# Performance work log

Hardware: AMD Instinct MI355X
Metric: run time of the kernel (lower is better)

The kernel has to match this reference:

```python
import jax, jax.numpy as jnp
import numpy as np

NUM_ANCHORS = 3
MAX_DETECTIONS = 10
CONF_THRESH = 0.5


def setup_inputs() -> dict:
    key = jax.random.key(0)
    k1, k2, k3 = jax.random.split(key, 3)
    B, T, D = 32, 512, 2048
    features = jax.random.normal(k1, (B, T, D), dtype=jnp.float32)
    W_bbox = jax.random.normal(k2, (D, NUM_ANCHORS * 4), dtype=jnp.float32) * 0.02
    b_bbox = jnp.zeros((NUM_ANCHORS * 4,), dtype=jnp.float32)
    W_conf = jax.random.normal(k3, (D, NUM_ANCHORS), dtype=jnp.float32) * 0.02
    b_conf = jnp.zeros((NUM_ANCHORS,), dtype=jnp.float32)
    return {"features": features, "W_bbox": W_bbox, "b_bbox": b_bbox,
            "W_conf": W_conf, "b_conf": b_conf}


def reference(features, W_bbox, b_bbox, W_conf, b_conf):
    # features: [B, T, D]
    B, T, D = features.shape
    A = NUM_ANCHORS
    k = min(MAX_DETECTIONS, A)  # = 3

    # Dual linear heads (the two trivial GEMMs)
    bbox_pred = (jnp.einsum('btd,df->btf', features, W_bbox) + b_bbox).reshape(B, T, A, 4)
    conf_pred = jax.nn.sigmoid(jnp.einsum('btd,da->bta', features, W_conf) + b_conf)  # [B,T,A]

    # Vectorized replacement of the per-(b,t) Python loop:
    # top-k over anchors, gather boxes, threshold mask -> padded output.
    topk_conf, topk_idx = jax.lax.top_k(conf_pred, k)                    # [B,T,k]
    topk_boxes = jnp.take_along_axis(bbox_pred, topk_idx[..., None], axis=2)  # [B,T,k,4]
    valid = topk_conf > CONF_THRESH                                      # [B,T,k]
    # Invalid slots zeroed: matches the original's "drop invalid / zeros fallback"
    # semantics in a fixed-shape padded representation.
    boxes_out = jnp.where(valid[..., None], topk_boxes, 0.0)
    return boxes_out, topk_conf, valid
```

## Files before the change

kernel.cpp:

```cpp
#include <hip/hip_runtime.h>
#include <math.h>


#define DCOLS 2048
#define RPB   64
#define NW    16
#define CHUNK (DCOLS / NW)
#define PSTR  15

__global__ __launch_bounds__(1024, 4)
void ped_det_kernel(const float* __restrict__ feat,
                    const float* __restrict__ Wb,
                    const float* __restrict__ bb,
                    const float* __restrict__ Wc,
                    const float* __restrict__ bc,
                    float* __restrict__ out,
                    int nrows)
{
    __shared__ float P[NW * RPB * PSTR];
    float* S = P;

    const int t    = threadIdx.x;
    const int lane = t & 63;
    const int w    = t >> 6;
    const int wu   = __builtin_amdgcn_readfirstlane(w);
    const int row  = blockIdx.x * RPB + lane;
    const int kb   = wu * CHUNK;

    float acc[15];
#pragma unroll
    for (int j = 0; j < 15; ++j) acc[j] = 0.0f;

    const float* fp = feat + (size_t)row * DCOLS;

#pragma unroll
    for (int g = 0; g < CHUNK / 16; ++g) {
        const int d0 = kb + g * 16;
        const float4 f0 = *(const float4*)(fp + d0 + 0);
        const float4 f1 = *(const float4*)(fp + d0 + 4);
        const float4 f2 = *(const float4*)(fp + d0 + 8);
        const float4 f3 = *(const float4*)(fp + d0 + 12);
        const float fv[16] = { f0.x, f0.y, f0.z, f0.w,
                               f1.x, f1.y, f1.z, f1.w,
                               f2.x, f2.y, f2.z, f2.w,
                               f3.x, f3.y, f3.z, f3.w };
#pragma unroll
        for (int q = 0; q < 4; ++q) {
            const int du = d0 + q * 4;
            const float* __restrict__ wbp = Wb + (size_t)du * 12;
            const float* __restrict__ wcp = Wc + (size_t)du * 3;
#pragma unroll
            for (int j = 0; j < 4; ++j) {
                const float v = fv[q * 4 + j];
                acc[0]  += v * wbp[j * 12 + 0];
                acc[1]  += v * wbp[j * 12 + 1];
                acc[2]  += v * wbp[j * 12 + 2];
                acc[3]  += v * wbp[j * 12 + 3];
                acc[4]  += v * wbp[j * 12 + 4];
                acc[5]  += v * wbp[j * 12 + 5];
                acc[6]  += v * wbp[j * 12 + 6];
                acc[7]  += v * wbp[j * 12 + 7];
                acc[8]  += v * wbp[j * 12 + 8];
                acc[9]  += v * wbp[j * 12 + 9];
                acc[10] += v * wbp[j * 12 + 10];
                acc[11] += v * wbp[j * 12 + 11];
                acc[12] += v * wcp[j * 3 + 0];
                acc[13] += v * wcp[j * 3 + 1];
                acc[14] += v * wcp[j * 3 + 2];
            }
        }
    }

    {
        float* pp = &P[(wu * RPB + lane) * PSTR];
#pragma unroll
        for (int j = 0; j < 15; ++j) pp[j] = acc[j];
    }
    __syncthreads();

    float sval = 0.0f;
    int rl = 0, jj = 0;
    if (t < RPB * 15) {
        rl = t / 15;
        jj = t % 15;
        float s = 0.0f;
#pragma unroll
        for (int w2 = 0; w2 < NW; ++w2)
            s += P[(w2 * RPB + rl) * PSTR + jj];
        s += (jj < 12) ? bb[jj] : bc[jj - 12];
        sval = s;
    }
    __syncthreads();

    if (t < RPB * 15)
        S[rl * 16 + jj] = sval;
    __syncthreads();

    if (t < RPB) {
        const int r2 = t;
        float box[12];
#pragma unroll
        for (int j = 0; j < 12; ++j) box[j] = S[r2 * 16 + j];
        float conf[3];
#pragma unroll
        for (int a = 0; a < 3; ++a)
            conf[a] = 1.0f / (1.0f + __expf(-S[r2 * 16 + 12 + a]));

        int i0 = 0; float m0 = conf[0];
        if (conf[1] > m0) { i0 = 1; m0 = conf[1]; }
        if (conf[2] > m0) { i0 = 2; m0 = conf[2]; }
        const int ra = (i0 == 0) ? 1 : 0;
        const int rb = (i0 == 2) ? 1 : 2;
        int i1, i2;
        if (conf[rb] > conf[ra]) { i1 = rb; i2 = ra; }
        else                     { i1 = ra; i2 = rb; }
        const int idx[3] = { i0, i1, i2 };

        const int ro = blockIdx.x * RPB + r2;
        float* boxout  = out + (size_t)ro * 12;
        float* confout = out + (size_t)nrows * 12 + (size_t)ro * 3;
        float* valout  = out + (size_t)nrows * 15 + (size_t)ro * 3;
#pragma unroll
        for (int sl = 0; sl < 3; ++sl) {
            const int   a   = idx[sl];
            const float cv  = conf[a];
            const bool  vld = cv > 0.5f;
            float4 bx;
            bx.x = vld ? box[a * 4 + 0] : 0.0f;
            bx.y = vld ? box[a * 4 + 1] : 0.0f;
            bx.z = vld ? box[a * 4 + 2] : 0.0f;
            bx.w = vld ? box[a * 4 + 3] : 0.0f;
            *(float4*)(boxout + sl * 4) = bx;
            confout[sl] = cv;
            valout[sl]  = vld ? 1.0f : 0.0f;
        }
    }
}

extern "C" void kernel_launch(void* const* d_in, const int* in_sizes, int n_in,
                              void* d_out, int out_size, void* d_ws, size_t ws_size,
                              hipStream_t stream) {
    const float* feat = (const float*)d_in[0];
    const float* Wb   = (const float*)d_in[1];
    const float* bb   = (const float*)d_in[2];
    const float* Wc   = (const float*)d_in[3];
    const float* bc   = (const float*)d_in[4];
    float* out = (float*)d_out;

    const int nrows   = in_sizes[0] / DCOLS;
    const int nblocks = nrows / RPB;

    ped_det_kernel<<<dim3(nblocks), dim3(1024), 0, stream>>>(
        feat, Wb, bb, Wc, bc, out, nrows);
}
```

Baseline: 40.59 us.

## Split-K GEMV with double-buffered global-to-LDS staging and separate epilogue kernel

Splits the feature reduction dimension in half across two blocks per 64-row tile, staging features through a swizzled double-buffered LDS tile loaded with direct global-to-LDS async loads. Partial sums go to workspace and a second kernel adds them, applies bias and sigmoid, and does the top-k selection and writes. The aim is coalesced, latency-hidden streaming of the 128MB feature tensor and more blocks in flight. The cost is an extra launch, a workspace round trip, and barriers on every chunk.

```diff
diff --git a/kernel.cpp b/kernel.cpp
--- a/kernel.cpp
+++ b/kernel.cpp
@@ -1,57 +1,79 @@
 #include <hip/hip_runtime.h>
 #include <math.h>
+#include <stdint.h>
 
 
 #define DCOLS 2048
 #define RPB   64
-#define NW    16
-#define CHUNK (DCOLS / NW)
-#define PSTR  15
+#define NWAVE 8
+#define KHALF 1024
+#define CCH   64
+#define NCH   (KHALF / CCH)
+#define TILEF (RPB * CCH)
 
-__global__ __launch_bounds__(1024, 4)
-void ped_det_kernel(const float* __restrict__ feat,
-                    const float* __restrict__ Wb,
-                    const float* __restrict__ bb,
-                    const float* __restrict__ Wc,
-                    const float* __restrict__ bc,
-                    float* __restrict__ out,
-                    int nrows)
+__global__ __launch_bounds__(512, 4)
+void ped_part_kernel(const float* __restrict__ feat,
+                     const float* __restrict__ Wb,
+                     const float* __restrict__ Wc,
+                     float* __restrict__ ws)
 {
-    __shared__ float P[NW * RPB * PSTR];
-    float* S = P;
+    __shared__ __align__(16) float lds[2][TILEF];
 
     const int t    = threadIdx.x;
     const int lane = t & 63;
     const int w    = t >> 6;
     const int wu   = __builtin_amdgcn_readfirstlane(w);
-    const int row  = blockIdx.x * RPB + lane;
-    const int kb   = wu * CHUNK;
+
+    const int half    = blockIdx.x & 1;
+    const int rowBase = (blockIdx.x >> 1) * RPB;
+    const int kbase   = half * KHALF;
+
+    const int rsub = lane >> 4;
+    const int su   = lane & 15;
 
     float acc[15];
 #pragma unroll
     for (int j = 0; j < 15; ++j) acc[j] = 0.0f;
 
-    const float* fp = feat + (size_t)row * DCOLS;
+    const float* fbase = feat + (size_t)rowBase * DCOLS + kbase;
 
+    auto STAGE = [&](int c, int p) {
 #pragma unroll
-    for (int g = 0; g < CHUNK / 16; ++g) {
-        const int d0 = kb + g * 16;
-        const float4 f0 = *(const float4*)(fp + d0 + 0);
-        const float4 f1 = *(const float4*)(fp + d0 + 4);
-        const float4 f2 = *(const float4*)(fp + d0 + 8);
-        const float4 f3 = *(const float4*)(fp + d0 + 12);
-        const float fv[16] = { f0.x, f0.y, f0.z, f0.w,
-                               f1.x, f1.y, f1.z, f1.w,
-                               f2.x, f2.y, f2.z, f2.w,
-                               f3.x, f3.y, f3.z, f3.w };
+        for (int i = 0; i < 2; ++i) {
+            const int r  = wu * 8 + i * 4 + rsub;
+            const int gs = su ^ (r & 7);
+            const float* g = fbase + (size_t)r * DCOLS + c * CCH + gs * 4;
+            const float* l = &lds[p][(wu * 8 + i * 4) * CCH];
+            __builtin_amdgcn_global_load_lds(
+                (const __attribute__((address_space(1))) void*)g,
+                (__attribute__((address_space(3))) void*)l, 16, 0, 0);
+        }
+    };
+
+    STAGE(0, 0);
+
+    for (int c = 0; c < NCH; ++c) {
+        if (c + 1 < NCH) {
+            STAGE(c + 1, (c + 1) & 1);
+            asm volatile("s_waitcnt vmcnt(2)" ::: "memory");
+        } else {
+            asm volatile("s_waitcnt vmcnt(0)" ::: "memory");
+        }
+        asm volatile("s_barrier" ::: "memory");
+
+        const float* buf = &lds[c & 1][0];
 #pragma unroll
-        for (int q = 0; q < 4; ++q) {
-            const int du = d0 + q * 4;
+        for (int q = 0; q < 2; ++q) {
+            const int s = wu * 2 + q;
+            const float4 f = *(const float4*)(buf + (size_t)lane * CCH
+                                              + ((s ^ (lane & 7)) << 2));
+            const int du = kbase + c * CCH + wu * 8 + q * 4;
             const float* __restrict__ wbp = Wb + (size_t)du * 12;
             const float* __restrict__ wcp = Wc + (size_t)du * 3;
+            const float fv[4] = { f.x, f.y, f.z, f.w };
 #pragma unroll
             for (int j = 0; j < 4; ++j) {
-                const float v = fv[q * 4 + j];
+                const float v = fv[j];
                 acc[0]  += v * wbp[j * 12 + 0];
                 acc[1]  += v * wbp[j * 12 + 1];
                 acc[2]  += v * wbp[j * 12 + 2];
@@ -69,71 +91,84 @@
                 acc[14] += v * wcp[j * 3 + 2];
             }
         }
+        asm volatile("s_waitcnt lgkmcnt(0)" ::: "memory");
+        asm volatile("s_barrier" ::: "memory");
     }
 
     {
-        float* pp = &P[(wu * RPB + lane) * PSTR];
+        float* P  = &lds[0][0];
+        float* pp = P + (size_t)(wu * RPB + lane) * 16;
 #pragma unroll
         for (int j = 0; j < 15; ++j) pp[j] = acc[j];
     }
     __syncthreads();
 
-    float sval = 0.0f;
-    int rl = 0, jj = 0;
-    if (t < RPB * 15) {
-        rl = t / 15;
-        jj = t % 15;
-        float s = 0.0f;
+    const float* P = &lds[0][0];
 #pragma unroll
-        for (int w2 = 0; w2 < NW; ++w2)
-            s += P[(w2 * RPB + rl) * PSTR + jj];
-        s += (jj < 12) ? bb[jj] : bc[jj - 12];
-        sval = s;
+    for (int u0 = 0; u0 < 2; ++u0) {
+        const int u = t + u0 * 512;
+        if (u < RPB * 15) {
+            const int r = u / 15;
+            const int j = u - r * 15;
+            float sum = 0.0f;
+#pragma unroll
+            for (int w2 = 0; w2 < NWAVE; ++w2)
+                sum += P[(size_t)(w2 * RPB + r) * 16 + j];
+            ws[((size_t)(rowBase + r) * 2 + half) * 16 + j] = sum;
+        }
     }
-    __syncthreads();
+}
 
-    if (t < RPB * 15)
-        S[rl * 16 + jj] = sval;
-    __syncthreads();
+__global__ __launch_bounds__(256, 4)
+void ped_epi_kernel(const float* __restrict__ ws,
+                    const float* __restrict__ bb,
+                    const float* __restrict__ bc,
+                    float* __restrict__ out, int nrows)
+{
+    const int r = blockIdx.x * 256 + threadIdx.x;
+    if (r >= nrows) return;
 
-    if (t < RPB) {
-        const int r2 = t;
-        float box[12];
+    const float* p = ws + (size_t)r * 32;
+    float s[15];
 #pragma unroll
-        for (int j = 0; j < 12; ++j) box[j] = S[r2 * 16 + j];
-        float conf[3];
+    for (int j = 0; j < 15; ++j)
+        s[j] = p[j] + p[16 + j] + ((j < 12) ? bb[j] : bc[j - 12]);
+
+    float conf[3];
 #pragma unroll
-        for (int a = 0; a < 3; ++a)
-            conf[a] = 1.0f / (1.0f + __expf(-S[r2 * 16 + 12 + a]));
+    for (int a = 0; a < 3; ++a)
+        conf[a] = 1.0f / (1.0f + __expf(-s[12 + a]));
 
-        int i0 = 0; float m0 = conf[0];
-        if (conf[1] > m0) { i0 = 1; m0 = conf[1]; }
-        if (conf[2] > m0) { i0 = 2; m0 = conf[2]; }
-        const int ra = (i0 == 0) ? 1 : 0;
-        const int rb = (i0 == 2) ? 1 : 2;
-        int i1, i2;
-        if (conf[rb] > conf[ra]) { i1 = rb; i2 = ra; }
-        else                     { i1 = ra; i2 = rb; }
-        const int idx[3] = { i0, i1, i2 };
+    int i0 = 0; float m0 = conf[0];
+    if (conf[1] > m0) { i0 = 1; m0 = conf[1]; }
+    if (conf[2] > m0) { i0 = 2; m0 = conf[2]; }
+    const int ra = (i0 == 0) ? 1 : 0;
+    const int rb = (i0 == 2) ? 1 : 2;
+    int i1, i2;
+    if (conf[rb] > conf[ra]) { i1 = rb; i2 = ra; }
+    else                     { i1 = ra; i2 = rb; }
+    const int idx[3] = { i0, i1, i2 };
 
-        const int ro = blockIdx.x * RPB + r2;
-        float* boxout  = out + (size_t)ro * 12;
-        float* confout = out + (size_t)nrows * 12 + (size_t)ro * 3;
-        float* valout  = out + (size_t)nrows * 15 + (size_t)ro * 3;
+    float* boxout  = out + (size_t)r * 12;
+    float* confout = out + (size_t)nrows * 12 + (size_t)r * 3;
+    float* valout  = out + (size_t)nrows * 15 + (size_t)r * 3;
 #pragma unroll
-        for (int sl = 0; sl < 3; ++sl) {
-            const int   a   = idx[sl];
-            const float cv  = conf[a];
-            const bool  vld = cv > 0.5f;
-            float4 bx;
-            bx.x = vld ? box[a * 4 + 0] : 0.0f;
-            bx.y = vld ? box[a * 4 + 1] : 0.0f;
-            bx.z = vld ? box[a * 4 + 2] : 0.0f;
-            bx.w = vld ? box[a * 4 + 3] : 0.0f;
-            *(float4*)(boxout + sl * 4) = bx;
-            confout[sl] = cv;
-            valout[sl]  = vld ? 1.0f : 0.0f;
-        }
+    for (int sl = 0; sl < 3; ++sl) {
+        const int   a   = idx[sl];
+        const float cv  = conf[a];
+        const bool  vld = cv > 0.5f;
+        const float b0 = (a == 0) ? s[0] : (a == 1) ? s[4]  : s[8];
+        const float b1 = (a == 0) ? s[1] : (a == 1) ? s[5]  : s[9];
+        const float b2 = (a == 0) ? s[2] : (a == 1) ? s[6]  : s[10];
+        const float b3 = (a == 0) ? s[3] : (a == 1) ? s[7]  : s[11];
+        float4 bx;
+        bx.x = vld ? b0 : 0.0f;
+        bx.y = vld ? b1 : 0.0f;
+        bx.z = vld ? b2 : 0.0f;
+        bx.w = vld ? b3 : 0.0f;
+        *(float4*)(boxout + sl * 4) = bx;
+        confout[sl] = cv;
+        valout[sl]  = vld ? 1.0f : 0.0f;
     }
 }
 
@@ -146,10 +181,12 @@
     const float* Wc   = (const float*)d_in[3];
     const float* bc   = (const float*)d_in[4];
     float* out = (float*)d_out;
+    float* ws  = (float*)d_ws;
 
-    const int nrows   = in_sizes[0] / DCOLS;
-    const int nblocks = nrows / RPB;
+    const int nrows = in_sizes[0] / DCOLS;
+    const int nb1   = (nrows / RPB) * 2;
 
-    ped_det_kernel<<<dim3(nblocks), dim3(1024), 0, stream>>>(
-        feat, Wb, bb, Wc, bc, out, nrows);
+    ped_part_kernel<<<dim3(nb1), dim3(512), 0, stream>>>(feat, Wb, Wc, ws);
+    ped_epi_kernel<<<dim3((nrows + 255) / 256), dim3(256), 0, stream>>>(
+        ws, bb, bc, out, nrows);
 }
```

Result: no change. 41.10 us (+1.2%).

## Stage feature tiles through LDS with async global_load_lds multi-buffering

Applied to the files above, without the earlier changes.

Replaces each lane's direct strided float4 loads of its own row with a 4-deep LDS ring of 64x64 tiles filled by global_load_lds. Each wave copies four rows coalesced, using an XOR swizzle, then reads its 4-column slice back from LDS. Manual vmcnt waits and barriers are meant to overlap the next tiles' loads with the current FMAs. In exchange it adds two block barriers per chunk across 32 chunks, raises LDS use to 64KB, which may cut occupancy, and re-reads weights with smaller per-iteration work.

```diff
diff --git a/kernel.cpp b/kernel.cpp
--- a/kernel.cpp
+++ b/kernel.cpp
@@ -1,11 +1,15 @@
 #include <hip/hip_runtime.h>
 #include <math.h>
+#include <stdint.h>
 
 
 #define DCOLS 2048
 #define RPB   64
 #define NW    16
-#define CHUNK (DCOLS / NW)
+#define CCH   64
+#define NCH   (DCOLS / CCH)
+#define NBUF  4
+#define TILEF (RPB * CCH)
 #define PSTR  15
 
 __global__ __launch_bounds__(1024, 4)
@@ -17,58 +21,80 @@
                     float* __restrict__ out,
                     int nrows)
 {
-    __shared__ float P[NW * RPB * PSTR];
+    __shared__ __align__(16) float lds[NBUF][TILEF];
+    float* P = &lds[0][0];
     float* S = P;
 
     const int t    = threadIdx.x;
     const int lane = t & 63;
     const int w    = t >> 6;
     const int wu   = __builtin_amdgcn_readfirstlane(w);
-    const int row  = blockIdx.x * RPB + lane;
-    const int kb   = wu * CHUNK;
+
+    const int rowBase = blockIdx.x * RPB;
+
+    const int rsub = lane >> 4;
+    const int su   = lane & 15;
+    const int rst  = wu * 4 + rsub;
+    const size_t gofs = (size_t)rst * DCOLS + ((su ^ (rst & 7)) << 2);
+    const float* fbase = feat + (size_t)rowBase * DCOLS;
+
+    auto STAGE = [&](int c, int p) {
+        const float* g = fbase + gofs + c * CCH;
+        const float* l = &lds[p][wu * 4 * CCH];
+        __builtin_amdgcn_global_load_lds(
+            (const __attribute__((address_space(1))) void*)g,
+            (__attribute__((address_space(3))) void*)l, 16, 0, 0);
+    };
+
+    const int roff = lane * CCH + ((wu ^ (lane & 7)) << 2);
 
     float acc[15];
 #pragma unroll
     for (int j = 0; j < 15; ++j) acc[j] = 0.0f;
 
-    const float* fp = feat + (size_t)row * DCOLS;
+    STAGE(0, 0);
+    STAGE(1, 1);
+    STAGE(2, 2);
 
+    for (int c = 0; c < NCH; ++c) {
+        if (c + 3 < NCH) STAGE(c + 3, (c + 3) & (NBUF - 1));
+
+        const int rem = NCH - 1 - c;
+        if (rem >= 3)      asm volatile("s_waitcnt vmcnt(3)" ::: "memory");
+        else if (rem == 2) asm volatile("s_waitcnt vmcnt(2)" ::: "memory");
+        else if (rem == 1) asm volatile("s_waitcnt vmcnt(1)" ::: "memory");
+        else               asm volatile("s_waitcnt vmcnt(0)" ::: "memory");
+        asm volatile("s_barrier" ::: "memory");
+
+        const float* buf = &lds[c & (NBUF - 1)][0];
+        const float4 f = *(const float4*)(buf + roff);
+
+        const int du = c * CCH + wu * 4;
+        const float* __restrict__ wbp = Wb + (size_t)du * 12;
+        const float* __restrict__ wcp = Wc + (size_t)du * 3;
+        const float fv[4] = { f.x, f.y, f.z, f.w };
 #pragma unroll
-    for (int g = 0; g < CHUNK / 16; ++g) {
-        const int d0 = kb + g * 16;
-        const float4 f0 = *(const float4*)(fp + d0 + 0);
-        const float4 f1 = *(const float4*)(fp + d0 + 4);
-        const float4 f2 = *(const float4*)(fp + d0 + 8);
-        const float4 f3 = *(const float4*)(fp + d0 + 12);
-        const float fv[16] = { f0.x, f0.y, f0.z, f0.w,
-                               f1.x, f1.y, f1.z, f1.w,
-                               f2.x, f2.y, f2.z, f2.w,
-                               f3.x, f3.y, f3.z, f3.w };
-#pragma unroll
-        for (int q = 0; q < 4; ++q) {
-            const int du = d0 + q * 4;
-            const float* __restrict__ wbp = Wb + (size_t)du * 12;
-            const float* __restrict__ wcp = Wc + (size_t)du * 3;
-#pragma unroll
-            for (int j = 0; j < 4; ++j) {
-                const float v = fv[q * 4 + j];
-                acc[0]  += v * wbp[j * 12 + 0];
-                acc[1]  += v * wbp[j * 12 + 1];
-                acc[2]  += v * wbp[j * 12 + 2];
-                acc[3]  += v * wbp[j * 12 + 3];
-                acc[4]  += v * wbp[j * 12 + 4];
-                acc[5]  += v * wbp[j * 12 + 5];
-                acc[6]  += v * wbp[j * 12 + 6];
-                acc[7]  += v * wbp[j * 12 + 7];
-                acc[8]  += v * wbp[j * 12 + 8];
-                acc[9]  += v * wbp[j * 12 + 9];
-                acc[10] += v * wbp[j * 12 + 10];
-                acc[11] += v * wbp[j * 12 + 11];
-                acc[12] += v * wcp[j * 3 + 0];
-                acc[13] += v * wcp[j * 3 + 1];
-                acc[14] += v * wcp[j * 3 + 2];
-            }
+        for (int j = 0; j < 4; ++j) {
+            const float v = fv[j];
+            acc[0]  += v * wbp[j * 12 + 0];
+            acc[1]  += v * wbp[j * 12 + 1];
+            acc[2]  += v * wbp[j * 12 + 2];
+            acc[3]  += v * wbp[j * 12 + 3];
+            acc[4]  += v * wbp[j * 12 + 4];
+            acc[5]  += v * wbp[j * 12 + 5];
+            acc[6]  += v * wbp[j * 12 + 6];
+            acc[7]  += v * wbp[j * 12 + 7];
+            acc[8]  += v * wbp[j * 12 + 8];
+            acc[9]  += v * wbp[j * 12 + 9];
+            acc[10] += v * wbp[j * 12 + 10];
+            acc[11] += v * wbp[j * 12 + 11];
+            acc[12] += v * wcp[j * 3 + 0];
+            acc[13] += v * wcp[j * 3 + 1];
+            acc[14] += v * wcp[j * 3 + 2];
         }
+
+        asm volatile("s_waitcnt lgkmcnt(0)" ::: "memory");
+        asm volatile("s_barrier" ::: "memory");
     }
 
     {
```

Result: no change. 40.06 us (-1.3%).

## Stage feature tiles through swizzled LDS with coalesced row loads and register prefetch

Applied to the files above, without the earlier changes.

Before, each lane streamed its own row, so every wave load was strided across 64 rows. Now each wave loads contiguous 1KB segments of four rows (fully coalesced float4 loads) and writes them into a 64x256 LDS tile with an XOR swizzle. Lanes then read their row's slice back from LDS with fewer bank conflicts. The next chunk is prefetched into registers while the current one is being computed, at the cost of extra syncthreads and a 64KB LDS footprint that may limit occupancy.

```diff
diff --git a/kernel.cpp b/kernel.cpp
--- a/kernel.cpp
+++ b/kernel.cpp
@@ -1,11 +1,14 @@
 #include <hip/hip_runtime.h>
 #include <math.h>
+#include <stdint.h>
 
 
 #define DCOLS 2048
 #define RPB   64
 #define NW    16
-#define CHUNK (DCOLS / NW)
+#define CCH   256
+#define NCH   (DCOLS / CCH)
+#define TILEF (RPB * CCH)
 #define PSTR  15
 
 __global__ __launch_bounds__(1024, 4)
@@ -17,60 +20,85 @@
                     float* __restrict__ out,
                     int nrows)
 {
-    __shared__ float P[NW * RPB * PSTR];
+    __shared__ __align__(16) float buf[TILEF];
+    float* P = &buf[0];
     float* S = P;
 
     const int t    = threadIdx.x;
     const int lane = t & 63;
     const int w    = t >> 6;
     const int wu   = __builtin_amdgcn_readfirstlane(w);
-    const int row  = blockIdx.x * RPB + lane;
-    const int kb   = wu * CHUNK;
+
+    const int rowBase = blockIdx.x * RPB;
+    const float* fbase = feat + (size_t)rowBase * DCOLS;
 
     float acc[15];
 #pragma unroll
     for (int j = 0; j < 15; ++j) acc[j] = 0.0f;
 
-    const float* fp = feat + (size_t)row * DCOLS;
+    float4 rg[4];
+
+    auto LOADC = [&](int c) {
+#pragma unroll
+        for (int i = 0; i < 4; ++i) {
+            const int r = wu * 4 + i;
+            rg[i] = *(const float4*)(fbase + (size_t)r * DCOLS
+                                     + c * CCH + (lane << 2));
+        }
+    };
+    auto DSWRITE = [&]() {
+#pragma unroll
+        for (int i = 0; i < 4; ++i) {
+            const int r = wu * 4 + i;
+            *(float4*)(&buf[(size_t)r * CCH + ((lane ^ (r & 7)) << 2)]) = rg[i];
+        }
+    };
+
+    LOADC(0);
+    DSWRITE();
+    __syncthreads();
+
+    for (int c = 0; c < NCH; ++c) {
+        if (c + 1 < NCH) LOADC(c + 1);
 
 #pragma unroll
-    for (int g = 0; g < CHUNK / 16; ++g) {
-        const int d0 = kb + g * 16;
-        const float4 f0 = *(const float4*)(fp + d0 + 0);
-        const float4 f1 = *(const float4*)(fp + d0 + 4);
-        const float4 f2 = *(const float4*)(fp + d0 + 8);
-        const float4 f3 = *(const float4*)(fp + d0 + 12);
-        const float fv[16] = { f0.x, f0.y, f0.z, f0.w,
-                               f1.x, f1.y, f1.z, f1.w,
-                               f2.x, f2.y, f2.z, f2.w,
-                               f3.x, f3.y, f3.z, f3.w };
-#pragma unroll
         for (int q = 0; q < 4; ++q) {
-            const int du = d0 + q * 4;
+            const int s = wu * 4 + q;
+            const float4 f = *(const float4*)(&buf[(size_t)lane * CCH
+                                              + ((s ^ (lane & 7)) << 2)]);
+            const int du = c * CCH + wu * 16 + q * 4;
             const float* __restrict__ wbp = Wb + (size_t)du * 12;
             const float* __restrict__ wcp = Wc + (size_t)du * 3;
+            const float fv[4] = { f.x, f.y, f.z, f.w };
 #pragma unroll
-            for (int j = 0; j < 4; ++j) {
-                const float v = fv[q * 4 + j];
-                acc[0]  += v * wbp[j * 12 + 0];
-                acc[1]  += v * wbp[j * 12 + 1];
-                acc[2]  += v * wbp[j * 12 + 2];
-                acc[3]  += v * wbp[j * 12 + 3];
-                acc[4]  += v * wbp[j * 12 + 4];
-                acc[5]  += v * wbp[j * 12 + 5];
-                acc[6]  += v * wbp[j * 12 + 6];
-                acc[7]  += v * wbp[j * 12 + 7];
-                acc[8]  += v * wbp[j * 12 + 8];
-                acc[9]  += v * wbp[j * 12 + 9];
-                acc[10] += v * wbp[j * 12 + 10];
-                acc[11] += v * wbp[j * 12 + 11];
-                acc[12] += v * wcp[j * 3 + 0];
-                acc[13] += v * wcp[j * 3 + 1];
-                acc[14] += v * wcp[j * 3 + 2];
+            for (int jj = 0; jj < 4; ++jj) {
+                const float v = fv[jj];
+                acc[0]  += v * wbp[jj * 12 + 0];
+                acc[1]  += v * wbp[jj * 12 + 1];
+                acc[2]  += v * wbp[jj * 12 + 2];
+                acc[3]  += v * wbp[jj * 12 + 3];
+                acc[4]  += v * wbp[jj * 12 + 4];
+                acc[5]  += v * wbp[jj * 12 + 5];
+                acc[6]  += v * wbp[jj * 12 + 6];
+                acc[7]  += v * wbp[jj * 12 + 7];
+                acc[8]  += v * wbp[jj * 12 + 8];
+                acc[9]  += v * wbp[jj * 12 + 9];
+                acc[10] += v * wbp[jj * 12 + 10];
+                acc[11] += v * wbp[jj * 12 + 11];
+                acc[12] += v * wcp[jj * 3 + 0];
+                acc[13] += v * wcp[jj * 3 + 1];
+                acc[14] += v * wcp[jj * 3 + 2];
             }
+        }
+
+        __syncthreads();
+        if (c + 1 < NCH) {
+            DSWRITE();
+            __syncthreads();
         }
     }
 
+    __syncthreads();
     {
         float* pp = &P[(wu * RPB + lane) * PSTR];
 #pragma unroll
```

Measured after the change: 83.94 us. +106.8%, slower.
